# Kernel tuning notes

Hardware: AMD Instinct MI355X
Metric: run time of the kernel (lower is better)

Reference implementation:

```python
import jax, jax.numpy as jnp
import numpy as np

# Model constants (from init_kwargs)
C, T, H = 64, 64, 12          # num_channels, temporal_len, num_heads
BLOCK_IDX = 0                 # even -> temporal attention within each channel
QMAX = 127.0                  # symmetric int8


def fq(x):
    """Per-tensor symmetric int8 fake quantize-dequantize (Int8ActPerTensorFloat /
    Int8WeightPerTensorFloat style) with straight-through estimator."""
    s = jnp.maximum(jnp.max(jnp.abs(x)), 1e-8) / QMAX
    q = jnp.clip(jnp.round(x / s), -128.0, QMAX) * s
    return x + jax.lax.stop_gradient(q - x)


def layernorm(x, g, b):
    m = jnp.mean(x, axis=-1, keepdims=True)
    v = jnp.var(x, axis=-1, keepdims=True)
    return (x - m) * jax.lax.rsqrt(v + 1e-5) * g + b


def setup_inputs() -> dict:
    key = jax.random.key(0)
    ks = jax.random.split(key, 6)
    D = 768
    B = 8
    w = lambda k, shape: jax.random.normal(k, shape, jnp.float32) * 0.02
    return {
        "x": jax.random.normal(ks[0], (B, C * T, D), jnp.float32),
        "ln1_g": jnp.ones((D,), jnp.float32), "ln1_b": jnp.zeros((D,), jnp.float32),
        "qkv_w": w(ks[1], (3 * D, D)), "qkv_b": jnp.zeros((3 * D,), jnp.float32),
        "proj_w": w(ks[2], (D, D)), "proj_b": jnp.zeros((D,), jnp.float32),
        "ln2_g": jnp.ones((D,), jnp.float32), "ln2_b": jnp.zeros((D,), jnp.float32),
        "fc1_w": w(ks[3], (4 * D, D)), "fc1_b": jnp.zeros((4 * D,), jnp.float32),
        "fc2_w": w(ks[4], (D, 4 * D)), "fc2_b": jnp.zeros((D,), jnp.float32),
    }


def _attn(h, qkv_w, qkv_b, proj_w, proj_b):
    B, N, D = h.shape
    dh = D // H
    scale = 1.0 / np.sqrt(dh).astype(np.float32)
    # quantized qkv projection (input already fake-quanted, weights per-tensor int8)
    qkv = h @ fq(qkv_w).T + qkv_b                      # [B, N, 3D]
    qkv = qkv.reshape(B, C, T, 3, H, dh)
    if BLOCK_IDX % 2 == 0:
        # temporal attention: attend over T within each channel
        q, k, v = [qkv[:, :, :, i].transpose(0, 1, 3, 2, 4) for i in range(3)]  # [B,C,H,T,dh]
        scores = jnp.einsum("bchtd,bchsd->bchts", q, k) * scale
        p = jax.nn.softmax(scores, axis=-1)
        o = jnp.einsum("bchts,bchsd->bchtd", p, v)     # [B,C,H,T,dh]
        o = o.transpose(0, 1, 3, 2, 4).reshape(B, N, D)
    else:
        # channel attention: attend over C within each time step
        q, k, v = [qkv[:, :, :, i].transpose(0, 2, 3, 1, 4) for i in range(3)]  # [B,T,H,C,dh]
        scores = jnp.einsum("bthcd,bthed->bthce", q, k) * scale
        p = jax.nn.softmax(scores, axis=-1)
        o = jnp.einsum("bthce,bthed->bthcd", p, v)
        o = o.transpose(0, 3, 1, 2, 4).reshape(B, N, D)
    # quantized output projection
    return fq(o) @ fq(proj_w).T + proj_b


def reference(x, ln1_g, ln1_b, qkv_w, qkv_b, proj_w, proj_b,
              ln2_g, ln2_b, fc1_w, fc1_b, fc2_w, fc2_b):
    # attn branch
    h = fq(layernorm(x, ln1_g, ln1_b))                 # post_norm1_quant
    x = _attn(h, qkv_w, qkv_b, proj_w, proj_b) + x     # add1 residual
    # mlp branch
    h = fq(layernorm(x, ln2_g, ln2_b))                 # post_norm2_quant
    h = jax.nn.gelu(h @ fq(fc1_w).T + fc1_b, approximate=False)
    h = fq(h)                                          # post_gelu_quant
    return h @ fq(fc2_w).T + fc2_b + x                 # add2 residual
```

## Files before the change

### kernel.cpp

```cpp
#include <hip/hip_runtime.h>
#include <cmath>
#include <cstdint>

typedef _Float16 f16;
typedef _Float16 half8 __attribute__((ext_vector_type(8)));
typedef _Float16 half4 __attribute__((ext_vector_type(4)));
typedef float f32x4 __attribute__((ext_vector_type(4)));
typedef int i32x4 __attribute__((ext_vector_type(4)));
typedef int8_t c8v __attribute__((ext_vector_type(8)));
typedef int8_t c4v __attribute__((ext_vector_type(4)));

#define M_TOTAL 32768
#define D_MODEL 768
#define NE_TOT  25165824
#define SPREAD_STRIDE 16


__device__ __forceinline__ void async_copy16(void* lds, const void* gmem) {
  __builtin_amdgcn_global_load_lds(
      (__attribute__((address_space(1))) void*)gmem,
      (__attribute__((address_space(3))) void*)lds, 16, 0, 0);
}

__device__ __forceinline__ float gelu_fast(float v) {
  float x = v * 0.70710678118654752f;
  float ax = fabsf(x);
  float t = __builtin_amdgcn_rcpf(fmaf(0.3275911f, ax, 1.0f));
  float y = t * (0.254829592f +
            t * (-0.284496736f +
            t * (1.421413741f +
            t * (-1.453152027f + t * 1.061405429f))));
  float e = __expf(-x * x);
  float erf_ax = fmaf(-y, e, 1.0f);
  float erf_x = copysignf(erf_ax, x);
  return 0.5f * v * (1.0f + erf_x);
}

__device__ __forceinline__ float slot_scale(const unsigned* slot) {
  return fmaxf(__uint_as_float(*slot), 1e-8f) / 127.0f;
}

__device__ __forceinline__ int8_t q8_val(float v, float s) {
  float q = fminf(fmaxf(rintf(v / s), -128.f), 127.f);
  return (int8_t)(int)q;
}

__device__ __forceinline__ float block_reduce_max(float m) {
  __shared__ float red_brm[4];
  for (int o = 32; o; o >>= 1) m = fmaxf(m, __shfl_down(m, o));
  int lane = threadIdx.x & 63, wv = threadIdx.x >> 6;
  if (lane == 0) red_brm[wv] = m;
  __syncthreads();
  return fmaxf(fmaxf(red_brm[0], red_brm[1]), fmaxf(red_brm[2], red_brm[3]));
}

__device__ __forceinline__ unsigned* spread_cell(unsigned* spread, int slot,
                                                 int cell) {
  return spread + slot * 64 * SPREAD_STRIDE + (cell & 63) * SPREAD_STRIDE;
}

__device__ __forceinline__ int xcd_swizzle(int lin, int nwg) {
  return (lin & 7) * (nwg >> 3) + (lin >> 3);
}

__device__ __forceinline__ void load_resid16(const float* resid, int N,
                                             int r0, int c0, float* rv) {
#pragma unroll
  for (int j = 0; j < 4; ++j)
#pragma unroll
    for (int reg = 0; reg < 4; ++reg)
      rv[j * 4 + reg] = resid[(size_t)(r0 + reg) * N + c0 + j * 16];
}


__global__ void zero_spread_k(unsigned* s) {
  int i = blockIdx.x * blockDim.x + threadIdx.x;
  if (i < 8 * 64 * SPREAD_STRIDE) s[i] = 0u;
}

__global__ void reduce_slots_k(const unsigned* __restrict__ spread,
                               unsigned* __restrict__ finals, int slot_lo,
                               int n_slots) {
  int wv = threadIdx.x >> 6, lane = threadIdx.x & 63;
  if (wv >= n_slots) return;
  int slot = slot_lo + wv;
  float m = __uint_as_float(spread[slot * 64 * SPREAD_STRIDE + lane * SPREAD_STRIDE]);
  for (int o = 32; o; o >>= 1) m = fmaxf(m, __shfl_down(m, o));
  if (lane == 0) finals[slot] = __float_as_uint(m);
}

__global__ __launch_bounds__(256) void absmax_k(const float* __restrict__ x,
                                                int n4, unsigned* spread,
                                                int slot) {
  int i = blockIdx.x * blockDim.x + threadIdx.x;
  int stride = gridDim.x * blockDim.x;
  float m = 0.f;
  const float4* x4 = (const float4*)x;
  for (; i < n4; i += stride) {
    float4 v = x4[i];
    m = fmaxf(m, fmaxf(fmaxf(fabsf(v.x), fabsf(v.y)),
                       fmaxf(fabsf(v.z), fabsf(v.w))));
  }
  m = block_reduce_max(m);
  if (threadIdx.x == 0)
    atomicMax(spread_cell(spread, slot, blockIdx.x), __float_as_uint(m));
}

__global__ void quant_w8_k(const float* __restrict__ x, int n4,
                           const unsigned* __restrict__ slot,
                           int8_t* __restrict__ out) {
  int i = blockIdx.x * blockDim.x + threadIdx.x;
  if (i >= n4) return;
  float s = slot_scale(slot);
  float4 v = ((const float4*)x)[i];
  c4v q = {q8_val(v.x, s), q8_val(v.y, s), q8_val(v.z, s), q8_val(v.w, s)};
  ((c4v*)out)[i] = q;
}

__global__ __launch_bounds__(256) void ln_k(const float* __restrict__ x,
                                            const float* __restrict__ gw,
                                            const float* __restrict__ bw,
                                            f16* __restrict__ out,
                                            unsigned* spread, int slot) {
  int tid = threadIdx.x, lane = tid & 63, wv = tid >> 6;
  int row = blockIdx.x * 4 + wv;
  const float4* xr = (const float4*)(x + (size_t)row * D_MODEL);
  float4 v[3];
  float s = 0.f, ss = 0.f;
#pragma unroll
  for (int j = 0; j < 3; ++j) {
    v[j] = xr[lane + j * 64];
    s += v[j].x + v[j].y + v[j].z + v[j].w;
    ss += v[j].x * v[j].x + v[j].y * v[j].y + v[j].z * v[j].z +
          v[j].w * v[j].w;
  }
#pragma unroll
  for (int o = 32; o; o >>= 1) {
    s += __shfl_xor(s, o);
    ss += __shfl_xor(ss, o);
  }
  float mean = s * (1.f / 768.f);
  float var = ss * (1.f / 768.f) - mean * mean;
  float rstd = rsqrtf(var + 1e-5f);
  const float4* g4 = (const float4*)gw;
  const float4* b4 = (const float4*)bw;
  f16* outr = out + (size_t)row * D_MODEL;
  float m = 0.f;
#pragma unroll
  for (int j = 0; j < 3; ++j) {
    float4 g = g4[lane + j * 64], b = b4[lane + j * 64];
    float y0 = (v[j].x - mean) * rstd * g.x + b.x;
    float y1 = (v[j].y - mean) * rstd * g.y + b.y;
    float y2 = (v[j].z - mean) * rstd * g.z + b.z;
    float y3 = (v[j].w - mean) * rstd * g.w + b.w;
    half4 hq = {(f16)y0, (f16)y1, (f16)y2, (f16)y3};
    *(half4*)(outr + (size_t)(lane + j * 64) * 4) = hq;
    m = fmaxf(m, fmaxf(fmaxf(fabsf(y0), fabsf(y1)),
                       fmaxf(fabsf(y2), fabsf(y3))));
  }
#pragma unroll
  for (int o = 32; o; o >>= 1) m = fmaxf(m, __shfl_xor(m, o));
  if (lane == 0)
    atomicMax(spread_cell(spread, slot, blockIdx.x * 4 + wv),
              __float_as_uint(m));
}

__global__ void quant8_k(const f16* __restrict__ src, int n8,
                         const unsigned* __restrict__ slot,
                         int8_t* __restrict__ out) {
  int i = blockIdx.x * blockDim.x + threadIdx.x;
  if (i >= n8) return;
  float s = slot_scale(slot);
  half8 v = ((const half8*)src)[i];
  c8v q;
#pragma unroll
  for (int j = 0; j < 8; ++j) q[j] = q8_val((float)v[j], s);
  ((c8v*)out)[i] = q;
}

__global__ void quant_strided8_k(const f16* __restrict__ src,
                                 const unsigned* __restrict__ slot,
                                 int8_t* __restrict__ out) {
  int i = blockIdx.x * blockDim.x + threadIdx.x;
  if (i >= NE_TOT / 8) return;
  int row = i / 96, c8 = i - row * 96;
  half8 v = *(const half8*)(src + (size_t)row * 2304 + c8 * 8);
  float s = slot_scale(slot);
  c8v q;
#pragma unroll
  for (int j = 0; j < 8; ++j) q[j] = q8_val((float)v[j], s);
  ((c8v*)out)[i] = q;
}

template <int MODE>
__global__ __launch_bounds__(256) void gemm_i8_t(
    const int8_t* __restrict__ A, const int8_t* __restrict__ B,
    const unsigned* __restrict__ slotA, const unsigned* __restrict__ slotB,
    const float* __restrict__ bias, const float* resid,
    float* outf, f16* outh, unsigned* spread, int slot,
    int N, int K) {
  __shared__ __attribute__((aligned(16))) int8_t sA[2][128 * 64];
  __shared__ __attribute__((aligned(16))) int8_t sB[2][128 * 64];
  int tid = threadIdx.x;
  int nwg = gridDim.x * gridDim.y;
  int lin = blockIdx.y * gridDim.x + blockIdx.x;
  int swz = xcd_swizzle(lin, nwg);
  int n0 = (swz % gridDim.x) * 128, m0 = (swz / gridDim.x) * 128;
  int lane = tid & 63, wv = tid >> 6;
  int wm = (wv & 1) * 64, wn = (wv >> 1) * 64;
  int lr = lane & 15, quad = lane >> 4;

  i32x4 acc[4][4];
#pragma unroll
  for (int i = 0; i < 4; ++i)
#pragma unroll
    for (int j = 0; j < 4; ++j) acc[i][j] = i32x4{0, 0, 0, 0};

  auto stage = [&](int buf, int k0) {
#pragma unroll
    for (int it = 0; it < 2; ++it) {
      int c = it * 256 + tid;
      int r = c >> 2;
      int sl = c & 3;
      int goff = (sl ^ (r & 3)) * 16;
      async_copy16(&sA[buf][c * 16], A + (size_t)(m0 + r) * K + k0 + goff);
      async_copy16(&sB[buf][c * 16], B + (size_t)(n0 + r) * K + k0 + goff);
    }
  };

  stage(0, 0);
  int nsteps = K >> 6;
  int cur = 0;
  for (int t = 0; t < nsteps; ++t) {
    if (t + 1 < nsteps) {
      stage(cur ^ 1, (t + 1) << 6);
      asm volatile("s_waitcnt vmcnt(4)" ::: "memory");
    } else {
      asm volatile("s_waitcnt vmcnt(0)" ::: "memory");
    }
    __builtin_amdgcn_s_barrier();
    i32x4 af[4], bfv[4];
#pragma unroll
    for (int i = 0; i < 4; ++i)
      af[i] = *(const i32x4*)
          &sA[cur][(wm + i * 16 + lr) * 64 + ((quad ^ (lr & 3)) * 16)];
#pragma unroll
    for (int j = 0; j < 4; ++j)
      bfv[j] = *(const i32x4*)
          &sB[cur][(wn + j * 16 + lr) * 64 + ((quad ^ (lr & 3)) * 16)];
#pragma unroll
    for (int i = 0; i < 4; ++i)
#pragma unroll
      for (int j = 0; j < 4; ++j)
        acc[i][j] = __builtin_amdgcn_mfma_i32_16x16x64_i8(af[i], bfv[j],
                                                          acc[i][j], 0, 0, 0);
    __builtin_amdgcn_s_barrier();
    cur ^= 1;
  }

  float scale = slot_scale(slotA) * slot_scale(slotB);
  int r0 = m0 + wm + quad * 4, c0 = n0 + wn + lr;
  float bv[4];
#pragma unroll
  for (int j = 0; j < 4; ++j) bv[j] = bias[c0 + j * 16];
  if (MODE == 2) {
    float rvA[16], rvB[16];
    load_resid16(resid, N, r0, c0, rvA);
#pragma unroll
    for (int i = 0; i < 4; ++i) {
      float* curv = (i & 1) ? rvB : rvA;
      float* nxt = (i & 1) ? rvA : rvB;
      if (i < 3) load_resid16(resid, N, r0 + (i + 1) * 16, c0, nxt);
#pragma unroll
      for (int j = 0; j < 4; ++j)
#pragma unroll
        for (int reg = 0; reg < 4; ++reg) {
          size_t idx = (size_t)(r0 + i * 16 + reg) * N + c0 + j * 16;
          outf[idx] = (float)acc[i][j][reg] * scale + bv[j] + curv[j * 4 + reg];
        }
    }
  } else if (MODE == 1) {
    float lmax = 0.f;
#pragma unroll
    for (int i = 0; i < 4; ++i)
#pragma unroll
      for (int j = 0; j < 4; ++j)
#pragma unroll
        for (int reg = 0; reg < 4; ++reg) {
          size_t idx = (size_t)(r0 + i * 16 + reg) * N + c0 + j * 16;
          float v = gelu_fast((float)acc[i][j][reg] * scale + bv[j]);
          lmax = fmaxf(lmax, fabsf(v));
          outh[idx] = (f16)v;
        }
    float bm = block_reduce_max(lmax);
    if (tid == 0)
      atomicMax(spread_cell(spread, slot, blockIdx.x + gridDim.x * blockIdx.y),
                __float_as_uint(bm));
  } else {
#pragma unroll
    for (int i = 0; i < 4; ++i)
#pragma unroll
      for (int j = 0; j < 4; ++j)
#pragma unroll
        for (int reg = 0; reg < 4; ++reg) {
          size_t idx = (size_t)(r0 + i * 16 + reg) * N + c0 + j * 16;
          outh[idx] = (f16)((float)acc[i][j][reg] * scale + bv[j]);
        }
  }
}

__global__ __launch_bounds__(256) void attn_k(f16* __restrict__ qkv,
                                              unsigned* spread, int slot) {
  __shared__ __attribute__((aligned(16))) f16 sQ[64 * 72];
  __shared__ __attribute__((aligned(16))) f16 sK[64 * 72];
  __shared__ __attribute__((aligned(16))) f16 sV[64 * 72];
  __shared__ __attribute__((aligned(16))) f16 sP[64 * 72];
  int tid = threadIdx.x, lane = tid & 63, wv = tid >> 6;
  int lr = lane & 15, quad = lane >> 4;
  int swz = xcd_swizzle(blockIdx.x, gridDim.x);
  int h = swz % 12, bc = swz / 12;
  size_t base = (size_t)bc * 64 * 2304;
  int qo = h * 64, ko = qo + 768, vo = qo + 1536;

#pragma unroll
  for (int p = 0; p < 2; ++p) {
    int idx = p * 256 + tid;
    int t = idx >> 3, d8 = idx & 7;
    size_t g = base + (size_t)t * 2304 + d8 * 8;
    *(half8*)&sQ[t * 72 + d8 * 8] = *(const half8*)(qkv + g + qo);
    *(half8*)&sK[t * 72 + d8 * 8] = *(const half8*)(qkv + g + ko);
    *(half8*)&sV[t * 72 + d8 * 8] = *(const half8*)(qkv + g + vo);
  }
  __syncthreads();

  f32x4 acc[4];
#pragma unroll
  for (int j = 0; j < 4; ++j) acc[j] = f32x4{0.f, 0.f, 0.f, 0.f};
#pragma unroll
  for (int ks = 0; ks < 2; ++ks) {
    half8 aq = *(const half8*)&sQ[(wv * 16 + lr) * 72 + ks * 32 + quad * 8];
#pragma unroll
    for (int j = 0; j < 4; ++j) {
      half8 bk = *(const half8*)&sK[(j * 16 + lr) * 72 + ks * 32 + quad * 8];
      acc[j] = __builtin_amdgcn_mfma_f32_16x16x32_f16(aq, bk, acc[j], 0, 0, 0);
    }
  }

  float pr[4][4];
#pragma unroll
  for (int reg = 0; reg < 4; ++reg) {
    float v0 = acc[0][reg] * 0.125f, v1 = acc[1][reg] * 0.125f;
    float v2 = acc[2][reg] * 0.125f, v3 = acc[3][reg] * 0.125f;
    float mx = fmaxf(fmaxf(v0, v1), fmaxf(v2, v3));
    for (int o = 8; o; o >>= 1) mx = fmaxf(mx, __shfl_xor(mx, o));
    float e0 = __expf(v0 - mx), e1 = __expf(v1 - mx);
    float e2 = __expf(v2 - mx), e3 = __expf(v3 - mx);
    float sum = e0 + e1 + e2 + e3;
    for (int o = 8; o; o >>= 1) sum += __shfl_xor(sum, o);
    float inv = 1.f / sum;
    pr[0][reg] = e0 * inv; pr[1][reg] = e1 * inv;
    pr[2][reg] = e2 * inv; pr[3][reg] = e3 * inv;
  }
#pragma unroll
  for (int j = 0; j < 4; ++j)
#pragma unroll
    for (int reg = 0; reg < 4; ++reg)
      sP[(wv * 16 + quad * 4 + reg) * 72 + j * 16 + lr] = (f16)pr[j][reg];
  __syncthreads();

  f32x4 oacc[4];
#pragma unroll
  for (int j = 0; j < 4; ++j) oacc[j] = f32x4{0.f, 0.f, 0.f, 0.f};
#pragma unroll
  for (int ks = 0; ks < 2; ++ks) {
    half8 ap = *(const half8*)&sP[(wv * 16 + lr) * 72 + ks * 32 + quad * 8];
#pragma unroll
    for (int j = 0; j < 4; ++j) {
      half8 bv;
#pragma unroll
      for (int jj = 0; jj < 8; ++jj)
        bv[jj] = sV[(ks * 32 + quad * 8 + jj) * 72 + j * 16 + lr];
      oacc[j] = __builtin_amdgcn_mfma_f32_16x16x32_f16(ap, bv, oacc[j], 0, 0, 0);
    }
  }

  float lmax = 0.f;
#pragma unroll
  for (int j = 0; j < 4; ++j)
#pragma unroll
    for (int reg = 0; reg < 4; ++reg) {
      int m = wv * 16 + quad * 4 + reg;
      float v = oacc[j][reg];
      qkv[base + (size_t)m * 2304 + qo + j * 16 + lr] = (f16)v;
      lmax = fmaxf(lmax, fabsf(v));
    }
  lmax = block_reduce_max(lmax);
  if (tid == 0)
    atomicMax(spread_cell(spread, slot, blockIdx.x), __float_as_uint(lmax));
}


extern "C" void kernel_launch(void* const* d_in, const int* in_sizes, int n_in,
                              void* d_out, int out_size, void* d_ws,
                              size_t ws_size, hipStream_t stream) {
  (void)in_sizes; (void)n_in; (void)out_size; (void)ws_size;
  const float* x      = (const float*)d_in[0];
  const float* ln1_g  = (const float*)d_in[1];
  const float* ln1_b  = (const float*)d_in[2];
  const float* qkv_w  = (const float*)d_in[3];
  const float* qkv_b  = (const float*)d_in[4];
  const float* proj_w = (const float*)d_in[5];
  const float* proj_b = (const float*)d_in[6];
  const float* ln2_g  = (const float*)d_in[7];
  const float* ln2_b  = (const float*)d_in[8];
  const float* fc1_w  = (const float*)d_in[9];
  const float* fc1_b  = (const float*)d_in[10];
  const float* fc2_w  = (const float*)d_in[11];
  const float* fc2_b  = (const float*)d_in[12];
  float* out = (float*)d_out;

  char* ws = (char*)d_ws;
  unsigned* spread = (unsigned*)ws;
  unsigned* finals = (unsigned*)(ws + 8 * 64 * SPREAD_STRIDE * 4);
  int8_t* qkv_wq  = (int8_t*)(ws + 33280);
  int8_t* proj_wq = qkv_wq + 1769472;
  int8_t* fc1_wq  = proj_wq + 589824;
  int8_t* fc2_wq  = fc1_wq + 2359296;
  int8_t* g_q  = fc2_wq + 2359296;
  f16*    hbuf = (f16*)g_q;
  int8_t* a_i8 = g_q + 50331648;
  f16*    big  = (f16*)(g_q + 100663296);

  zero_spread_k<<<(8 * 64 * SPREAD_STRIDE + 255) / 256, 256, 0, stream>>>(spread);

  absmax_k<<<256, 256, 0, stream>>>(qkv_w, 1769472 / 4, spread, 1);
  absmax_k<<<256, 256, 0, stream>>>(proj_w, 589824 / 4, spread, 2);
  absmax_k<<<256, 256, 0, stream>>>(fc1_w, 2359296 / 4, spread, 3);
  absmax_k<<<256, 256, 0, stream>>>(fc2_w, 2359296 / 4, spread, 4);
  reduce_slots_k<<<1, 256, 0, stream>>>(spread, finals, 1, 4);
  quant_w8_k<<<(1769472 / 4 + 255) / 256, 256, 0, stream>>>(qkv_w, 1769472 / 4, finals + 1, qkv_wq);
  quant_w8_k<<<(589824 / 4 + 255) / 256, 256, 0, stream>>>(proj_w, 589824 / 4, finals + 2, proj_wq);
  quant_w8_k<<<(2359296 / 4 + 255) / 256, 256, 0, stream>>>(fc1_w, 2359296 / 4, finals + 3, fc1_wq);
  quant_w8_k<<<(2359296 / 4 + 255) / 256, 256, 0, stream>>>(fc2_w, 2359296 / 4, finals + 4, fc2_wq);

  ln_k<<<8192, 256, 0, stream>>>(x, ln1_g, ln1_b, hbuf, spread, 0);
  reduce_slots_k<<<1, 64, 0, stream>>>(spread, finals, 0, 1);
  quant8_k<<<NE_TOT / 8 / 256, 256, 0, stream>>>(hbuf, NE_TOT / 8, finals + 0, a_i8);
  gemm_i8_t<0><<<dim3(18, 256), 256, 0, stream>>>(a_i8, qkv_wq, finals + 0, finals + 1,
                                                  qkv_b, nullptr, nullptr, big,
                                                  nullptr, 0, 2304, 768);
  attn_k<<<6144, 256, 0, stream>>>(big, spread, 5);
  reduce_slots_k<<<1, 64, 0, stream>>>(spread, finals, 5, 1);
  quant_strided8_k<<<NE_TOT / 8 / 256, 256, 0, stream>>>(big, finals + 5, a_i8);
  gemm_i8_t<2><<<dim3(6, 256), 256, 0, stream>>>(a_i8, proj_wq, finals + 5, finals + 2,
                                                 proj_b, x, out, nullptr,
                                                 nullptr, 0, 768, 768);
  ln_k<<<8192, 256, 0, stream>>>(out, ln2_g, ln2_b, hbuf, spread, 6);
  reduce_slots_k<<<1, 64, 0, stream>>>(spread, finals, 6, 1);
  quant8_k<<<NE_TOT / 8 / 256, 256, 0, stream>>>(hbuf, NE_TOT / 8, finals + 6, a_i8);
  gemm_i8_t<1><<<dim3(24, 256), 256, 0, stream>>>(a_i8, fc1_wq, finals + 6, finals + 3,
                                                  fc1_b, nullptr, nullptr, big,
                                                  spread, 7, 3072, 768);
  reduce_slots_k<<<1, 64, 0, stream>>>(spread, finals, 7, 1);
  quant8_k<<<100663296 / 8 / 256, 256, 0, stream>>>(big, 100663296 / 8, finals + 7, g_q);
  gemm_i8_t<2><<<dim3(6, 256), 256, 0, stream>>>(g_q, fc2_wq, finals + 7, finals + 4,
                                                 fc2_b, out, out, nullptr,
                                                 nullptr, 0, 768, 3072);
}
```

Measured before the change: 841.5 us.

## Triple-buffer A tiles in LDS and load B fragments directly to registers

Restructures the int8 GEMM main loop. Only A goes through LDS now, in three buffers with a paired-row swizzled layout. B fragments are read straight from global memory into double-buffered registers, and the loop is unrolled by two with hand-tuned vmcnt waits. The aim is to halve LDS traffic and staging work and to prefetch deeper so more memory latency is hidden, at the cost of uncoalesced direct global loads for B, more register pressure, and a loop that assumes an even step count.

```diff
diff --git a/kernel.cpp b/kernel.cpp
--- a/kernel.cpp
+++ b/kernel.cpp
@@ -20,6 +20,10 @@
   __builtin_amdgcn_global_load_lds(
       (__attribute__((address_space(1))) void*)gmem,
       (__attribute__((address_space(3))) void*)lds, 16, 0, 0);
+}
+
+__device__ __forceinline__ void issue_fence() {
+  asm volatile("" ::: "memory");
 }
 
 __device__ __forceinline__ float gelu_fast(float v) {
@@ -199,8 +203,7 @@
     const float* __restrict__ bias, const float* resid,
     float* outf, f16* outh, unsigned* spread, int slot,
     int N, int K) {
-  __shared__ __attribute__((aligned(16))) int8_t sA[2][128 * 64];
-  __shared__ __attribute__((aligned(16))) int8_t sB[2][128 * 64];
+  __shared__ __attribute__((aligned(16))) int8_t sT[3][64 * 128];
   int tid = threadIdx.x;
   int nwg = gridDim.x * gridDim.y;
   int lin = blockIdx.y * gridDim.x + blockIdx.x;
@@ -216,46 +219,94 @@
 #pragma unroll
     for (int j = 0; j < 4; ++j) acc[i][j] = i32x4{0, 0, 0, 0};
 
-  auto stage = [&](int buf, int k0) {
-#pragma unroll
-    for (int it = 0; it < 2; ++it) {
-      int c = it * 256 + tid;
-      int r = c >> 2;
-      int sl = c & 3;
-      int goff = (sl ^ (r & 3)) * 16;
-      async_copy16(&sA[buf][c * 16], A + (size_t)(m0 + r) * K + k0 + goff);
-      async_copy16(&sB[buf][c * 16], B + (size_t)(n0 + r) * K + k0 + goff);
-    }
+  auto mkA = [&](int c) {
+    int pr = c >> 3, sl = c & 7, g = sl ^ (pr & 7);
+    return A + (size_t)(m0 + pr * 2 + (g >> 2)) * K + (g & 3) * 16;
   };
-
-  stage(0, 0);
+  const int8_t* srcA0 = mkA(tid);
+  const int8_t* srcA1 = mkA(256 + tid);
+  int ld0 = tid * 16, ld1 = (256 + tid) * 16;
+  auto stageA = [&](int8_t* buf) {
+    async_copy16(buf + ld0, srcA0);
+    async_copy16(buf + ld1, srcA1);
+    srcA0 += 64;
+    srcA1 += 64;
+  };
+
+  const int8_t* Bp[4];
+#pragma unroll
+  for (int j = 0; j < 4; ++j)
+    Bp[j] = B + (size_t)(n0 + wn + j * 16 + lr) * K + quad * 16;
+  i32x4 bA[4], bB[4];
+  auto loadB = [&](i32x4* bf) {
+#pragma unroll
+    for (int j = 0; j < 4; ++j) {
+      bf[j] = *(const i32x4*)Bp[j];
+      Bp[j] += 64;
+    }
+  };
+
+  int aoff[4];
+#pragma unroll
+  for (int i = 0; i < 4; ++i) {
+    int r = wm + i * 16 + lr, pr = r >> 1;
+    aoff[i] = pr * 128 + ((((r & 1) << 2) | quad) ^ (pr & 7)) * 16;
+  }
+  auto compute = [&](const int8_t* s, const i32x4* bf) {
+    i32x4 af[4];
+#pragma unroll
+    for (int i = 0; i < 4; ++i) af[i] = *(const i32x4*)&s[aoff[i]];
+#pragma unroll
+    for (int i = 0; i < 4; ++i)
+#pragma unroll
+      for (int j = 0; j < 4; ++j)
+        acc[i][j] = __builtin_amdgcn_mfma_i32_16x16x64_i8(af[i], bf[j],
+                                                          acc[i][j], 0, 0, 0);
+  };
+
+  int8_t* cb0 = sT[0];
+  int8_t* cb1 = sT[1];
+  int8_t* cb2 = sT[2];
+  stageA(cb0);
+  issue_fence();
+  loadB(bA);
+  issue_fence();
+  stageA(cb1);
+  issue_fence();
   int nsteps = K >> 6;
-  int cur = 0;
-  for (int t = 0; t < nsteps; ++t) {
-    if (t + 1 < nsteps) {
-      stage(cur ^ 1, (t + 1) << 6);
-      asm volatile("s_waitcnt vmcnt(4)" ::: "memory");
+  int pairs = nsteps >> 1;
+  for (int S = 0; S < pairs; ++S) {
+    int t0 = 2 * S;
+    loadB(bB);
+    issue_fence();
+    if (t0 + 2 < nsteps) {
+      stageA(cb2);
+      asm volatile("s_waitcnt vmcnt(8)" ::: "memory");
+    } else {
+      asm volatile("s_waitcnt vmcnt(6)" ::: "memory");
+    }
+    __builtin_amdgcn_s_barrier();
+    compute(cb0, bA);
+    __builtin_amdgcn_s_barrier();
+    if (t0 + 2 < nsteps) {
+      loadB(bA);
+      issue_fence();
+    }
+    if (t0 + 3 < nsteps) {
+      stageA(cb0);
+      asm volatile("s_waitcnt vmcnt(8)" ::: "memory");
+    } else if (t0 + 2 < nsteps) {
+      asm volatile("s_waitcnt vmcnt(6)" ::: "memory");
     } else {
       asm volatile("s_waitcnt vmcnt(0)" ::: "memory");
     }
     __builtin_amdgcn_s_barrier();
-    i32x4 af[4], bfv[4];
-#pragma unroll
-    for (int i = 0; i < 4; ++i)
-      af[i] = *(const i32x4*)
-          &sA[cur][(wm + i * 16 + lr) * 64 + ((quad ^ (lr & 3)) * 16)];
-#pragma unroll
-    for (int j = 0; j < 4; ++j)
-      bfv[j] = *(const i32x4*)
-          &sB[cur][(wn + j * 16 + lr) * 64 + ((quad ^ (lr & 3)) * 16)];
-#pragma unroll
-    for (int i = 0; i < 4; ++i)
-#pragma unroll
-      for (int j = 0; j < 4; ++j)
-        acc[i][j] = __builtin_amdgcn_mfma_i32_16x16x64_i8(af[i], bfv[j],
-                                                          acc[i][j], 0, 0, 0);
+    compute(cb1, bB);
     __builtin_amdgcn_s_barrier();
-    cur ^= 1;
+    int8_t* tmp = cb0;
+    cb0 = cb2;
+    cb2 = cb1;
+    cb1 = tmp;
   }
 
   float scale = slot_scale(slotA) * slot_scale(slotB);
```

After: 989.2 us. 17.6% more time.

## Enlarge int8 GEMM tile to 256x128 with 512 threads and triple-buffered LDS

Applied to the files above, without the earlier changes.

Rework the int8 MFMA GEMM so each block uses 8 waves and covers a 256x128 output tile instead of 128x128, and halve the grid accordingly. The LDS staging becomes a three-buffer ring with two k-steps per loop iteration, using a new XOR-swizzled paired-row layout. The aim is more reuse of each B tile per block and deeper prefetch to hide global latency. The cost is higher LDS use (72KB) and register pressure, which may reduce occupancy. A templated block reduction now handles 8 waves.

```diff
diff --git a/kernel.cpp b/kernel.cpp
--- a/kernel.cpp
+++ b/kernel.cpp
@@ -45,13 +45,17 @@
   return (int8_t)(int)q;
 }
 
-__device__ __forceinline__ float block_reduce_max(float m) {
-  __shared__ float red_brm[4];
+template <int NW>
+__device__ __forceinline__ float block_reduce_max_t(float m) {
+  __shared__ float red_brm[NW];
   for (int o = 32; o; o >>= 1) m = fmaxf(m, __shfl_down(m, o));
   int lane = threadIdx.x & 63, wv = threadIdx.x >> 6;
   if (lane == 0) red_brm[wv] = m;
   __syncthreads();
-  return fmaxf(fmaxf(red_brm[0], red_brm[1]), fmaxf(red_brm[2], red_brm[3]));
+  float r = red_brm[0];
+#pragma unroll
+  for (int w = 1; w < NW; ++w) r = fmaxf(r, red_brm[w]);
+  return r;
 }
 
 __device__ __forceinline__ unsigned* spread_cell(unsigned* spread, int slot,
@@ -101,7 +105,7 @@
     m = fmaxf(m, fmaxf(fmaxf(fabsf(v.x), fabsf(v.y)),
                        fmaxf(fabsf(v.z), fabsf(v.w))));
   }
-  m = block_reduce_max(m);
+  m = block_reduce_max_t<4>(m);
   if (threadIdx.x == 0)
     atomicMax(spread_cell(spread, slot, blockIdx.x), __float_as_uint(m));
 }
@@ -193,21 +197,21 @@
 }
 
 template <int MODE>
-__global__ __launch_bounds__(256) void gemm_i8_t(
+__global__ __launch_bounds__(512) void gemm_i8_t(
     const int8_t* __restrict__ A, const int8_t* __restrict__ B,
     const unsigned* __restrict__ slotA, const unsigned* __restrict__ slotB,
     const float* __restrict__ bias, const float* resid,
     float* outf, f16* outh, unsigned* spread, int slot,
     int N, int K) {
-  __shared__ __attribute__((aligned(16))) int8_t sA[2][128 * 64];
-  __shared__ __attribute__((aligned(16))) int8_t sB[2][128 * 64];
+  __shared__ __attribute__((aligned(16))) int8_t sA[3][128 * 128];
+  __shared__ __attribute__((aligned(16))) int8_t sB[3][64 * 128];
   int tid = threadIdx.x;
   int nwg = gridDim.x * gridDim.y;
   int lin = blockIdx.y * gridDim.x + blockIdx.x;
   int swz = xcd_swizzle(lin, nwg);
-  int n0 = (swz % gridDim.x) * 128, m0 = (swz / gridDim.x) * 128;
+  int n0 = (swz % gridDim.x) * 128, m0 = (swz / gridDim.x) * 256;
   int lane = tid & 63, wv = tid >> 6;
-  int wm = (wv & 1) * 64, wn = (wv >> 1) * 64;
+  int wm = (wv >> 1) * 64, wn = (wv & 1) * 64;
   int lr = lane & 15, quad = lane >> 4;
 
   i32x4 acc[4][4];
@@ -216,46 +220,78 @@
 #pragma unroll
     for (int j = 0; j < 4; ++j) acc[i][j] = i32x4{0, 0, 0, 0};
 
-  auto stage = [&](int buf, int k0) {
-#pragma unroll
-    for (int it = 0; it < 2; ++it) {
-      int c = it * 256 + tid;
-      int r = c >> 2;
-      int sl = c & 3;
-      int goff = (sl ^ (r & 3)) * 16;
-      async_copy16(&sA[buf][c * 16], A + (size_t)(m0 + r) * K + k0 + goff);
-      async_copy16(&sB[buf][c * 16], B + (size_t)(n0 + r) * K + k0 + goff);
+  auto mkA = [&](int c) {
+    int pr = c >> 3, sl = c & 7, g = sl ^ (pr & 7);
+    return A + (size_t)(m0 + 2 * pr + (g >> 2)) * K + (g & 3) * 16;
+  };
+  auto mkB = [&](int c) {
+    int pr = c >> 3, sl = c & 7, g = sl ^ (pr & 7);
+    return B + (size_t)(n0 + 2 * pr + (g >> 2)) * K + (g & 3) * 16;
+  };
+  const int8_t* sa0 = mkA(tid);
+  const int8_t* sa1 = mkA(512 + tid);
+  const int8_t* sb0 = mkB(tid);
+  int la0 = tid * 16, la1 = (512 + tid) * 16;
+  auto stage = [&](int b) {
+    async_copy16(&sA[b][la0], sa0);
+    async_copy16(&sA[b][la1], sa1);
+    async_copy16(&sB[b][la0], sb0);
+    sa0 += 64;
+    sa1 += 64;
+    sb0 += 64;
+  };
+
+  int aoff[4], boff[4];
+#pragma unroll
+  for (int i = 0; i < 4; ++i) {
+    int r = wm + i * 16 + lr, pr = r >> 1;
+    aoff[i] = pr * 128 + (((((r & 1) << 2) | quad) ^ (pr & 7)) * 16);
+    int rb = wn + i * 16 + lr, prb = rb >> 1;
+    boff[i] = prb * 128 + (((((rb & 1) << 2) | quad) ^ (prb & 7)) * 16);
+  }
+  auto compute = [&](const int8_t* a_s, const int8_t* b_s) {
+    i32x4 af[4], bfv[4];
+#pragma unroll
+    for (int i = 0; i < 4; ++i) af[i] = *(const i32x4*)&a_s[aoff[i]];
+#pragma unroll
+    for (int j = 0; j < 4; ++j) bfv[j] = *(const i32x4*)&b_s[boff[j]];
+#pragma unroll
+    for (int i = 0; i < 4; ++i)
+#pragma unroll
+      for (int j = 0; j < 4; ++j)
+        acc[i][j] = __builtin_amdgcn_mfma_i32_16x16x64_i8(af[i], bfv[j],
+                                                          acc[i][j], 0, 0, 0);
+  };
+
+  int bi0 = 0, bi1 = 1, bi2 = 2;
+  stage(bi0);
+  stage(bi1);
+  int nsteps = K >> 6;
+  int pairs = nsteps >> 1;
+  for (int S = 0; S < pairs; ++S) {
+    bool last = (S == pairs - 1);
+    if (!last) {
+      stage(bi2);
+      asm volatile("s_waitcnt vmcnt(6)" ::: "memory");
+    } else {
+      asm volatile("s_waitcnt vmcnt(3)" ::: "memory");
     }
-  };
-
-  stage(0, 0);
-  int nsteps = K >> 6;
-  int cur = 0;
-  for (int t = 0; t < nsteps; ++t) {
-    if (t + 1 < nsteps) {
-      stage(cur ^ 1, (t + 1) << 6);
-      asm volatile("s_waitcnt vmcnt(4)" ::: "memory");
+    __builtin_amdgcn_s_barrier();
+    compute(sA[bi0], sB[bi0]);
+    __builtin_amdgcn_s_barrier();
+    if (!last) {
+      stage(bi0);
+      asm volatile("s_waitcnt vmcnt(6)" ::: "memory");
     } else {
       asm volatile("s_waitcnt vmcnt(0)" ::: "memory");
     }
     __builtin_amdgcn_s_barrier();
-    i32x4 af[4], bfv[4];
-#pragma unroll
-    for (int i = 0; i < 4; ++i)
-      af[i] = *(const i32x4*)
-          &sA[cur][(wm + i * 16 + lr) * 64 + ((quad ^ (lr & 3)) * 16)];
-#pragma unroll
-    for (int j = 0; j < 4; ++j)
-      bfv[j] = *(const i32x4*)
-          &sB[cur][(wn + j * 16 + lr) * 64 + ((quad ^ (lr & 3)) * 16)];
-#pragma unroll
-    for (int i = 0; i < 4; ++i)
-#pragma unroll
-      for (int j = 0; j < 4; ++j)
-        acc[i][j] = __builtin_amdgcn_mfma_i32_16x16x64_i8(af[i], bfv[j],
-                                                          acc[i][j], 0, 0, 0);
+    compute(sA[bi1], sB[bi1]);
     __builtin_amdgcn_s_barrier();
-    cur ^= 1;
+    int t = bi0;
+    bi0 = bi2;
+    bi2 = bi1;
+    bi1 = t;
   }
 
   float scale = slot_scale(slotA) * slot_scale(slotB);
@@ -292,7 +328,7 @@
           lmax = fmaxf(lmax, fabsf(v));
           outh[idx] = (f16)v;
         }
-    float bm = block_reduce_max(lmax);
+    float bm = block_reduce_max_t<8>(lmax);
     if (tid == 0)
       atomicMax(spread_cell(spread, slot, blockIdx.x + gridDim.x * blockIdx.y),
                 __float_as_uint(bm));
@@ -394,7 +430,7 @@
       qkv[base + (size_t)m * 2304 + qo + j * 16 + lr] = (f16)v;
       lmax = fmaxf(lmax, fabsf(v));
     }
-  lmax = block_reduce_max(lmax);
+  lmax = block_reduce_max_t<4>(lmax);
   if (tid == 0)
     atomicMax(spread_cell(spread, slot, blockIdx.x), __float_as_uint(lmax));
 }
@@ -446,24 +482,24 @@
   ln_k<<<8192, 256, 0, stream>>>(x, ln1_g, ln1_b, hbuf, spread, 0);
   reduce_slots_k<<<1, 64, 0, stream>>>(spread, finals, 0, 1);
   quant8_k<<<NE_TOT / 8 / 256, 256, 0, stream>>>(hbuf, NE_TOT / 8, finals + 0, a_i8);
-  gemm_i8_t<0><<<dim3(18, 256), 256, 0, stream>>>(a_i8, qkv_wq, finals + 0, finals + 1,
+  gemm_i8_t<0><<<dim3(18, 128), 512, 0, stream>>>(a_i8, qkv_wq, finals + 0, finals + 1,
                                                   qkv_b, nullptr, nullptr, big,
                                                   nullptr, 0, 2304, 768);
   attn_k<<<6144, 256, 0, stream>>>(big, spread, 5);
   reduce_slots_k<<<1, 64, 0, stream>>>(spread, finals, 5, 1);
   quant_strided8_k<<<NE_TOT / 8 / 256, 256, 0, stream>>>(big, finals + 5, a_i8);
-  gemm_i8_t<2><<<dim3(6, 256), 256, 0, stream>>>(a_i8, proj_wq, finals + 5, finals + 2,
+  gemm_i8_t<2><<<dim3(6, 128), 512, 0, stream>>>(a_i8, proj_wq, finals + 5, finals + 2,
                                                  proj_b, x, out, nullptr,
                                                  nullptr, 0, 768, 768);
   ln_k<<<8192, 256, 0, stream>>>(out, ln2_g, ln2_b, hbuf, spread, 6);
   reduce_slots_k<<<1, 64, 0, stream>>>(spread, finals, 6, 1);
   quant8_k<<<NE_TOT / 8 / 256, 256, 0, stream>>>(hbuf, NE_TOT / 8, finals + 6, a_i8);
-  gemm_i8_t<1><<<dim3(24, 256), 256, 0, stream>>>(a_i8, fc1_wq, finals + 6, finals + 3,
+  gemm_i8_t<1><<<dim3(24, 128), 512, 0, stream>>>(a_i8, fc1_wq, finals + 6, finals + 3,
                                                   fc1_b, nullptr, nullptr, big,
                                                   spread, 7, 3072, 768);
   reduce_slots_k<<<1, 64, 0, stream>>>(spread, finals, 7, 1);
   quant8_k<<<100663296 / 8 / 256, 256, 0, stream>>>(big, 100663296 / 8, finals + 7, g_q);
-  gemm_i8_t<2><<<dim3(6, 256), 256, 0, stream>>>(g_q, fc2_wq, finals + 7, finals + 4,
+  gemm_i8_t<2><<<dim3(6, 128), 512, 0, stream>>>(g_q, fc2_wq, finals + 7, finals + 4,
                                                  fc2_b, out, out, nullptr,
                                                  nullptr, 0, 768, 3072);
 }
```

Result: faster. 807.9 us (-4.0%).
